# Kernel tuning notes

Measured on AMD Instinct MI355X. Metric: run time of the kernel, lower is better.

Reference implementation:

```python
import jax, jax.numpy as jnp
import numpy as np

B, R, S = 4, 16384, 96

def setup_inputs() -> dict:
    key = jax.random.key(0)
    k1, k2, k3, k4 = jax.random.split(key, 4)
    colors = jax.random.normal(k1, (B, R, S, 3), dtype=jnp.float32)
    densities = jax.random.normal(k2, (B, R, S, 1), dtype=jnp.float32)
    # depths must be monotonically increasing along the sample axis
    depths = jnp.sort(jax.random.uniform(k3, (B, R, S, 1), dtype=jnp.float32), axis=2)
    sample_coordinates = jax.random.uniform(k4, (B, R, S, 3), dtype=jnp.float32)
    return {"colors": colors, "densities": densities, "depths": depths,
            "sample_coordinates": sample_coordinates, "white_back": 0}


def reference(colors, densities, depths, sample_coordinates, white_back):
    deltas = depths[:, :, 1:] - depths[:, :, :-1]                     # [B,R,S-1,1]
    colors_mid = (colors[:, :, :-1] + colors[:, :, 1:]) * 0.5
    densities_mid = (densities[:, :, :-1] + densities[:, :, 1:]) * 0.5
    depths_mid = (depths[:, :, :-1] + depths[:, :, 1:]) * 0.5
    coords_mid = (sample_coordinates[:, :, :-1] + sample_coordinates[:, :, 1:]) * 0.5

    densities_mid = jax.nn.softplus(densities_mid)                    # activation_factory
    alpha = 1.0 - jnp.exp(-densities_mid * deltas)                    # [B,R,S-1,1]

    ones = jnp.ones_like(alpha[:, :, :1])
    alpha_shifted = jnp.concatenate([ones, 1.0 - alpha + 1e-10], axis=-2)
    trans = jnp.cumprod(alpha_shifted, axis=-2)[:, :, :-1]            # transmittance T_i

    weights = alpha * trans                                            # [B,R,S-1,1]
    tau = trans[:, :, -1, :]                                           # [B,R,1]

    composite_rgb = jnp.sum(weights * colors_mid, axis=-2)             # [B,R,3]
    composite_point = jnp.sum(weights * coords_mid, axis=-2)           # [B,R,3]
    weight_total = jnp.sum(weights, axis=2)                            # [B,R,1]

    composite_depth = jnp.sum(weights * depths_mid, axis=-2)           # [B,R,1]
    composite_depth = jnp.nan_to_num(composite_depth, nan=jnp.inf)
    composite_depth = jnp.clip(composite_depth, jnp.min(depths), jnp.max(depths))

    composite_rgb = jnp.where(white_back != 0,
                              composite_rgb + 1.0 - weight_total,
                              composite_rgb)
    return composite_rgb, composite_depth, weights, composite_point, tau
```

## Files before the change

### kernel.cpp

```cpp
#include <hip/hip_runtime.h>
#include <hip/hip_bf16.h>

#define NRAYS 65536
#define NS    96
#define NI    95

#define OFF_RGB   0
#define OFF_DEPTH 196608
#define OFF_W     262144
#define OFF_PT    6488064
#define OFF_TAU   6684672

__global__ void init_minmax(unsigned* ws) {
    ws[0] = 0x7f800000u;
    ws[1] = 0u;
}

__global__ void depth_minmax(const float* __restrict__ deps, unsigned* ws) {
    int g = blockIdx.x * blockDim.x + threadIdx.x;
    float lo = deps[(size_t)g * NS];
    float hi = deps[(size_t)g * NS + NS - 1];
    #pragma unroll
    for (int off = 32; off; off >>= 1) {
        lo = fminf(lo, __shfl_xor(lo, off, 64));
        hi = fmaxf(hi, __shfl_xor(hi, off, 64));
    }
    if ((threadIdx.x & 63) == 0) {
        atomicMin(&ws[0], __float_as_uint(lo));
        atomicMax(&ws[1], __float_as_uint(hi));
    }
}

__device__ __forceinline__ float softplus_f(float x) {
    return fmaxf(x, 0.0f) + log1pf(__expf(-fabsf(x)));
}

__launch_bounds__(256)
__global__ void raymarch(const float* __restrict__ colors,
                         const float* __restrict__ dens,
                         const float* __restrict__ deps,
                         const float* __restrict__ coords,
                         const int* __restrict__ wbp,
                         const unsigned* __restrict__ mm,
                         float* __restrict__ out) {
    __shared__ float4 sC4[288];
    __shared__ float4 sP4[288];
    __shared__ float4 sD4[96];
    __shared__ float4 sZ4[96];
    __shared__ float  sF[4 * NS];

    const int tid  = threadIdx.x;
    const int w    = tid >> 6;
    const int lane = tid & 63;
    const int g    = blockIdx.x * 4 + w;

    {
        const float4* C4 = (const float4*)(colors + (size_t)blockIdx.x * (4 * NS * 3));
        const float4* P4 = (const float4*)(coords + (size_t)blockIdx.x * (4 * NS * 3));
        const float4* D4 = (const float4*)(dens   + (size_t)blockIdx.x * (4 * NS));
        const float4* Z4 = (const float4*)(deps   + (size_t)blockIdx.x * (4 * NS));
        for (int i = tid; i < 288; i += 256) { sC4[i] = C4[i]; sP4[i] = P4[i]; }
        if (tid < 96) { sD4[tid] = D4[tid]; sZ4[tid] = Z4[tid]; }
    }
    __syncthreads();

    const float* C = (const float*)sC4 + w * (NS * 3);
    const float* P = (const float*)sP4 + w * (NS * 3);
    const float* D = (const float*)sD4 + w * NS;
    const float* Z = (const float*)sZ4 + w * NS;
    float*       F = sF + w * NS;

    const int  i0 = 2 * lane, i1 = 2 * lane + 1;
    const bool v0 = (i0 < NI), v1 = (i1 < NI);

    int s = v0 ? i0 : 0;
    float za = Z[s], zb = Z[s + 1];
    float sp = softplus_f(0.5f * (D[s] + D[s + 1]));
    float E  = __expf(-sp * (zb - za));
    float a0 = v0 ? (1.0f - E) : 0.0f;
    float f0 = v0 ? (E + 1e-10f) : 1.0f;
    float dm0  = 0.5f * (za + zb);
    float cm0x = 0.5f * (C[3*s] + C[3*s+3]);
    float cm0y = 0.5f * (C[3*s+1] + C[3*s+4]);
    float cm0z = 0.5f * (C[3*s+2] + C[3*s+5]);
    float pm0x = 0.5f * (P[3*s] + P[3*s+3]);
    float pm0y = 0.5f * (P[3*s+1] + P[3*s+4]);
    float pm0z = 0.5f * (P[3*s+2] + P[3*s+5]);

    s = v1 ? i1 : 0;
    za = Z[s]; zb = Z[s + 1];
    sp = softplus_f(0.5f * (D[s] + D[s + 1]));
    E  = __expf(-sp * (zb - za));
    float a1 = v1 ? (1.0f - E) : 0.0f;
    float f1 = v1 ? (E + 1e-10f) : 1.0f;
    float dm1  = 0.5f * (za + zb);
    float cm1x = 0.5f * (C[3*s] + C[3*s+3]);
    float cm1y = 0.5f * (C[3*s+1] + C[3*s+4]);
    float cm1z = 0.5f * (C[3*s+2] + C[3*s+5]);
    float pm1x = 0.5f * (P[3*s] + P[3*s+3]);
    float pm1y = 0.5f * (P[3*s+1] + P[3*s+4]);
    float pm1z = 0.5f * (P[3*s+2] + P[3*s+5]);

    if (v0) F[i0] = f0;
    if (v1) F[i1] = f1;
    __syncthreads();

    float p = 1.0f, t0 = 1.0f, t1 = 1.0f, tau = 1.0f;
    for (int j = 0; j < NI; ++j) {
        if (j == i0) t0 = p;
        if (j == i1) t1 = p;
        if (j == NI - 1) tau = p;
        p *= F[j];
    }

    float w0 = a0 * t0, w1 = a1 * t1;

    {
        size_t wb = (size_t)OFF_W + (size_t)g * NI;
        if (v0) out[wb + i0] = w0;
        if (v1) out[wb + i1] = w1;
    }

    float acc[8];
    acc[0] = w0 * cm0x + w1 * cm1x;
    acc[1] = w0 * cm0y + w1 * cm1y;
    acc[2] = w0 * cm0z + w1 * cm1z;
    acc[3] = w0 * pm0x + w1 * pm1x;
    acc[4] = w0 * pm0y + w1 * pm1y;
    acc[5] = w0 * pm0z + w1 * pm1z;
    acc[6] = w0 * dm0  + w1 * dm1;
    acc[7] = w0 + w1;
    #pragma unroll
    for (int k = 0; k < 8; ++k) {
        #pragma unroll
        for (int off = 32; off; off >>= 1)
            acc[k] += __shfl_xor(acc[k], off, 64);
    }

    if (lane == 0) {
        float add = (wbp != nullptr && wbp[0] != 0) ? (1.0f - acc[7]) : 0.0f;
        size_t rb = (size_t)OFF_RGB + (size_t)g * 3;
        out[rb + 0] = acc[0] + add;
        out[rb + 1] = acc[1] + add;
        out[rb + 2] = acc[2] + add;
        size_t pb = (size_t)OFF_PT + (size_t)g * 3;
        out[pb + 0] = acc[3];
        out[pb + 1] = acc[4];
        out[pb + 2] = acc[5];
        float cd = acc[6];
        if (cd != cd) cd = __int_as_float(0x7f800000);
        float dmin = __uint_as_float(mm[0]);
        float dmax = __uint_as_float(mm[1]);
        cd = fminf(fmaxf(cd, dmin), dmax);
        out[OFF_DEPTH + g] = cd;
        out[OFF_TAU + g]   = tau;
    }
}

extern "C" void kernel_launch(void* const* d_in, const int* in_sizes, int n_in,
                              void* d_out, int out_size, void* d_ws, size_t ws_size,
                              hipStream_t stream) {
    const float* colors = nullptr; const float* coords = nullptr;
    const float* dens = nullptr;   const float* deps = nullptr;
    const int* wb = nullptr;
    int big = 0, small = 0;
    for (int i = 0; i < n_in; ++i) {
        if (in_sizes[i] == 4718592)      { if (big++ == 0) colors = (const float*)d_in[i]; else coords = (const float*)d_in[i]; }
        else if (in_sizes[i] == 1572864) { if (small++ == 0) dens = (const float*)d_in[i]; else deps = (const float*)d_in[i]; }
        else if (in_sizes[i] == 1)       { wb = (const int*)d_in[i]; }
    }
    if (!colors || !coords || !dens || !deps) {
        colors = (const float*)d_in[0];
        dens   = (const float*)d_in[1];
        deps   = (const float*)d_in[2];
        coords = (const float*)d_in[3];
        wb     = (n_in > 4) ? (const int*)d_in[4] : nullptr;
    }
    float* out = (float*)d_out;
    unsigned* mm = (unsigned*)d_ws;

    init_minmax<<<1, 1, 0, stream>>>(mm);
    depth_minmax<<<NRAYS / 256, 256, 0, stream>>>(deps, mm);
    raymarch<<<NRAYS / 4, 256, 0, stream>>>(colors, dens, deps, coords, wb, mm, out);
}
```

Before: 246.1 us.

## Replace shared-memory serial scan with register loads and wavefront shuffle scan

```diff
diff --git a/kernel.cpp b/kernel.cpp
--- a/kernel.cpp
+++ b/kernel.cpp
@@ -11,15 +11,18 @@
 #define OFF_PT    6488064
 #define OFF_TAU   6684672
 
-__global__ void init_minmax(unsigned* ws) {
-    ws[0] = 0x7f800000u;
-    ws[1] = 0u;
-}
-
-__global__ void depth_minmax(const float* __restrict__ deps, unsigned* ws) {
-    int g = blockIdx.x * blockDim.x + threadIdx.x;
-    float lo = deps[(size_t)g * NS];
-    float hi = deps[(size_t)g * NS + NS - 1];
+__global__ void depth_minmax_full(const float* __restrict__ deps, unsigned* ws) {
+    const int nt = gridDim.x * blockDim.x;
+    int t = blockIdx.x * blockDim.x + threadIdx.x;
+    float lo = __int_as_float(0x7f800000);
+    float hi = 0.0f;
+    const float4* Z4 = (const float4*)deps;
+    const int n4 = NRAYS * NS / 4;
+    for (int i = t; i < n4; i += nt) {
+        float4 z = Z4[i];
+        lo = fminf(lo, fminf(fminf(z.x, z.y), fminf(z.z, z.w)));
+        hi = fmaxf(hi, fmaxf(fmaxf(z.x, z.y), fmaxf(z.z, z.w)));
+    }
     #pragma unroll
     for (int off = 32; off; off >>= 1) {
         lo = fminf(lo, __shfl_xor(lo, off, 64));
@@ -31,8 +34,8 @@
     }
 }
 
-__device__ __forceinline__ float softplus_f(float x) {
-    return fmaxf(x, 0.0f) + log1pf(__expf(-fabsf(x)));
+__device__ __forceinline__ float softplus_fast(float x) {
+    return fmaxf(x, 0.0f) + __logf(1.0f + __expf(-fabsf(x)));
 }
 
 __launch_bounds__(256)
@@ -43,82 +46,67 @@
                          const int* __restrict__ wbp,
                          const unsigned* __restrict__ mm,
                          float* __restrict__ out) {
-    __shared__ float4 sC4[288];
-    __shared__ float4 sP4[288];
-    __shared__ float4 sD4[96];
-    __shared__ float4 sZ4[96];
-    __shared__ float  sF[4 * NS];
+    const int lane = threadIdx.x & 63;
+    const int g = blockIdx.x * 4 + (threadIdx.x >> 6);
 
-    const int tid  = threadIdx.x;
-    const int w    = tid >> 6;
-    const int lane = tid & 63;
-    const int g    = blockIdx.x * 4 + w;
+    const bool v0 = (lane <= 47);
+    const bool v1 = (lane <= 46);
+
+    float2 dp = make_float2(0.f, 0.f);
+    float2 dn = make_float2(0.f, 0.f);
+    float2 c01 = make_float2(0.f, 0.f), c23 = make_float2(0.f, 0.f),
+           c45 = make_float2(0.f, 0.f);
+    float2 p01 = make_float2(0.f, 0.f), p23 = make_float2(0.f, 0.f),
+           p45 = make_float2(0.f, 0.f);
+    if (v0) {
+        const float2* dpp = (const float2*)(deps + (size_t)g * NS);
+        const float2* dnp = (const float2*)(dens + (size_t)g * NS);
+        dp = dpp[lane];
+        dn = dnp[lane];
+        const float2* cp = (const float2*)(colors + (size_t)g * NS * 3);
+        c01 = cp[3 * lane + 0]; c23 = cp[3 * lane + 1]; c45 = cp[3 * lane + 2];
+        const float2* pp = (const float2*)(coords + (size_t)g * NS * 3);
+        p01 = pp[3 * lane + 0]; p23 = pp[3 * lane + 1]; p45 = pp[3 * lane + 2];
+    }
+    const int src = (lane < 63) ? lane + 1 : 63;
+    float d2  = __shfl(dp.x, src, 64);
+    float n2  = __shfl(dn.x, src, 64);
+    float cx2 = __shfl(c01.x, src, 64);
+    float cy2 = __shfl(c01.y, src, 64);
+    float cz2 = __shfl(c23.x, src, 64);
+    float px2 = __shfl(p01.x, src, 64);
+    float py2 = __shfl(p01.y, src, 64);
+    float pz2 = __shfl(p23.x, src, 64);
+
+    float E0 = __expf(-softplus_fast(0.5f * (dn.x + dn.y)) * (dp.y - dp.x));
+    float a0 = v0 ? (1.0f - E0) : 0.0f;
+    float f0 = v0 ? (E0 + 1e-10f) : 1.0f;
+    float E1 = __expf(-softplus_fast(0.5f * (dn.y + n2)) * (d2 - dp.y));
+    float a1 = v1 ? (1.0f - E1) : 0.0f;
+    float f1 = v1 ? (E1 + 1e-10f) : 1.0f;
+
+    float incl = f0 * f1;
+    #pragma unroll
+    for (int off = 1; off < 64; off <<= 1) {
+        float t = __shfl_up(incl, off, 64);
+        if (lane >= off) incl *= t;
+    }
+    float excl = __shfl_up(incl, 1, 64);
+    if (lane == 0) excl = 1.0f;
+    float w0 = a0 * excl;
+    float w1 = a1 * (excl * f0);
+    float tau = __shfl(excl, 47, 64);
+
+    float dm0 = 0.5f * (dp.x + dp.y), dm1 = 0.5f * (dp.y + d2);
+    float cm0x = 0.5f * (c01.x + c23.y), cm0y = 0.5f * (c01.y + c45.x), cm0z = 0.5f * (c23.x + c45.y);
+    float cm1x = 0.5f * (c23.y + cx2),   cm1y = 0.5f * (c45.x + cy2),   cm1z = 0.5f * (c45.y + cz2);
+    float pm0x = 0.5f * (p01.x + p23.y), pm0y = 0.5f * (p01.y + p45.x), pm0z = 0.5f * (p23.x + p45.y);
+    float pm1x = 0.5f * (p23.y + px2),   pm1y = 0.5f * (p45.x + py2),   pm1z = 0.5f * (p45.y + pz2);
 
     {
-        const float4* C4 = (const float4*)(colors + (size_t)blockIdx.x * (4 * NS * 3));
-        const float4* P4 = (const float4*)(coords + (size_t)blockIdx.x * (4 * NS * 3));
-        const float4* D4 = (const float4*)(dens   + (size_t)blockIdx.x * (4 * NS));
-        const float4* Z4 = (const float4*)(deps   + (size_t)blockIdx.x * (4 * NS));
-        for (int i = tid; i < 288; i += 256) { sC4[i] = C4[i]; sP4[i] = P4[i]; }
-        if (tid < 96) { sD4[tid] = D4[tid]; sZ4[tid] = Z4[tid]; }
-    }
-    __syncthreads();
-
-    const float* C = (const float*)sC4 + w * (NS * 3);
-    const float* P = (const float*)sP4 + w * (NS * 3);
-    const float* D = (const float*)sD4 + w * NS;
-    const float* Z = (const float*)sZ4 + w * NS;
-    float*       F = sF + w * NS;
-
-    const int  i0 = 2 * lane, i1 = 2 * lane + 1;
-    const bool v0 = (i0 < NI), v1 = (i1 < NI);
-
-    int s = v0 ? i0 : 0;
-    float za = Z[s], zb = Z[s + 1];
-    float sp = softplus_f(0.5f * (D[s] + D[s + 1]));
-    float E  = __expf(-sp * (zb - za));
-    float a0 = v0 ? (1.0f - E) : 0.0f;
-    float f0 = v0 ? (E + 1e-10f) : 1.0f;
-    float dm0  = 0.5f * (za + zb);
-    float cm0x = 0.5f * (C[3*s] + C[3*s+3]);
-    float cm0y = 0.5f * (C[3*s+1] + C[3*s+4]);
-    float cm0z = 0.5f * (C[3*s+2] + C[3*s+5]);
-    float pm0x = 0.5f * (P[3*s] + P[3*s+3]);
-    float pm0y = 0.5f * (P[3*s+1] + P[3*s+4]);
-    float pm0z = 0.5f * (P[3*s+2] + P[3*s+5]);
-
-    s = v1 ? i1 : 0;
-    za = Z[s]; zb = Z[s + 1];
-    sp = softplus_f(0.5f * (D[s] + D[s + 1]));
-    E  = __expf(-sp * (zb - za));
-    float a1 = v1 ? (1.0f - E) : 0.0f;
-    float f1 = v1 ? (E + 1e-10f) : 1.0f;
-    float dm1  = 0.5f * (za + zb);
-    float cm1x = 0.5f * (C[3*s] + C[3*s+3]);
-    float cm1y = 0.5f * (C[3*s+1] + C[3*s+4]);
-    float cm1z = 0.5f * (C[3*s+2] + C[3*s+5]);
-    float pm1x = 0.5f * (P[3*s] + P[3*s+3]);
-    float pm1y = 0.5f * (P[3*s+1] + P[3*s+4]);
-    float pm1z = 0.5f * (P[3*s+2] + P[3*s+5]);
-
-    if (v0) F[i0] = f0;
-    if (v1) F[i1] = f1;
-    __syncthreads();
-
-    float p = 1.0f, t0 = 1.0f, t1 = 1.0f, tau = 1.0f;
-    for (int j = 0; j < NI; ++j) {
-        if (j == i0) t0 = p;
-        if (j == i1) t1 = p;
-        if (j == NI - 1) tau = p;
-        p *= F[j];
-    }
-
-    float w0 = a0 * t0, w1 = a1 * t1;
-
-    {
-        size_t wb = (size_t)OFF_W + (size_t)g * NI;
-        if (v0) out[wb + i0] = w0;
-        if (v1) out[wb + i1] = w1;
+        size_t wb = (size_t)OFF_W + (size_t)g * NI + 2 * lane;
+        if (v0) out[wb]     = w0;
+        if (v1) out[wb + 1] = w1;
     }
 
     float acc[8];
@@ -160,26 +148,16 @@
 extern "C" void kernel_launch(void* const* d_in, const int* in_sizes, int n_in,
                               void* d_out, int out_size, void* d_ws, size_t ws_size,
                               hipStream_t stream) {
-    const float* colors = nullptr; const float* coords = nullptr;
-    const float* dens = nullptr;   const float* deps = nullptr;
-    const int* wb = nullptr;
-    int big = 0, small = 0;
-    for (int i = 0; i < n_in; ++i) {
-        if (in_sizes[i] == 4718592)      { if (big++ == 0) colors = (const float*)d_in[i]; else coords = (const float*)d_in[i]; }
-        else if (in_sizes[i] == 1572864) { if (small++ == 0) dens = (const float*)d_in[i]; else deps = (const float*)d_in[i]; }
-        else if (in_sizes[i] == 1)       { wb = (const int*)d_in[i]; }
-    }
-    if (!colors || !coords || !dens || !deps) {
-        colors = (const float*)d_in[0];
-        dens   = (const float*)d_in[1];
-        deps   = (const float*)d_in[2];
-        coords = (const float*)d_in[3];
-        wb     = (n_in > 4) ? (const int*)d_in[4] : nullptr;
-    }
+    const float* colors = (const float*)d_in[0];
+    const float* dens   = (const float*)d_in[1];
+    const float* deps   = (const float*)d_in[2];
+    const float* coords = (const float*)d_in[3];
+    const int*   wb     = (n_in > 4) ? (const int*)d_in[4] : nullptr;
     float* out = (float*)d_out;
     unsigned* mm = (unsigned*)d_ws;
 
-    init_minmax<<<1, 1, 0, stream>>>(mm);
-    depth_minmax<<<NRAYS / 256, 256, 0, stream>>>(deps, mm);
+    hipMemsetAsync(mm, 0xFF, 4, stream);
+    hipMemsetAsync(mm + 1, 0x00, 4, stream);
+    depth_minmax_full<<<256, 256, 0, stream>>>(deps, mm);
     raymarch<<<NRAYS / 4, 256, 0, stream>>>(colors, dens, deps, coords, wb, mm, out);
 }
```

After: 244.7 us. No clear change (-0.6%).
